# Kernel tuning notes

Hardware: AMD Instinct MI355X
Metric: run time of the kernel (lower is better)

## Reference

```python
import jax, jax.numpy as jnp
import numpy as np

B, S, D, DH, H, NCLS, VOCAB, L = 16, 512, 512, 512, 8, 10000, 32000, 6
HD = DH // H  # 64


def _norm(X, gamma, beta, axis):
    # torch.var is unbiased by default -> ddof=1
    mu = jnp.mean(X, axis=axis, keepdims=True)
    var = jnp.var(X, axis=axis, ddof=1, keepdims=True)
    return gamma * ((X - mu) / jnp.sqrt(var + 1e-8)) + beta


def _pos_table(s, d):
    pos = np.arange(s, dtype=np.float64)[:, None]
    i = np.arange(d, dtype=np.float64)[None, :]
    angle = pos / np.power(10000.0, (i - (i % 2)) / d)
    tab = np.where((np.arange(d)[None, :] % 2) == 0, np.sin(angle), np.cos(angle))
    return jnp.asarray(tab, dtype=jnp.float32)


def _encoder(x, p):
    b, s, d = x.shape

    def heads(w):
        y = x @ w.T                         # [B,S,DH]
        y = y.reshape(b, s, HD, H)          # interleaved split: channel c -> head c%8
        return jnp.transpose(y, (3, 0, 1, 2))  # [H,B,S,HD]

    q, k, v = heads(p['WQ']), heads(p['WK']), heads(p['WV'])
    # scaling uses d_k = x.shape[-1] = hidden_dim (not head_dim), as in source
    e = jnp.einsum('hbsd,hbtd->hbst', q, k) / jnp.sqrt(jnp.float32(d))
    e = _norm(e, p['ga'].reshape(H, 1, 1, 1), p['ba'].reshape(H, 1, 1, 1), axis=3)
    alpha = jax.nn.softmax(e, axis=3)
    head = jnp.einsum('hbst,hbtd->hbsd', alpha, v)      # [H,B,S,HD]
    a = jnp.transpose(head, (1, 2, 0, 3)).reshape(b, s, DH)  # cat(head[0..7], dim=2)
    attn = a @ p['WO']                                   # [B,S,D]
    x2 = _norm(attn + x, p['g1'], p['b1n'], axis=2)
    ff = jax.nn.relu(x2 @ p['W1'] + p['b1']) @ p['W2'] + p['b2']
    return _norm(ff + x2, p['g2'], p['b2n'], axis=2)


def setup_inputs() -> dict:
    key = jax.random.key(0)
    ks = jax.random.split(key, 16)
    sc = 0.05  # scale randn params for numerical stability across 6 layers
    return {
        'x': jax.random.randint(ks[0], (B, S), 0, VOCAB),
        'embedded_matrix': jax.random.normal(ks[1], (VOCAB, D), jnp.float32) * sc,
        'WQ': jax.random.normal(ks[2], (L, DH, D), jnp.float32) * sc,
        'WK': jax.random.normal(ks[3], (L, DH, D), jnp.float32) * sc,
        'WV': jax.random.normal(ks[4], (L, DH, D), jnp.float32) * sc,
        'WO': jax.random.normal(ks[5], (L, DH, D), jnp.float32) * sc,
        'W1': jax.random.normal(ks[6], (L, D, 4 * D), jnp.float32) * sc,
        'b1': jax.random.normal(ks[7], (L, 4 * D), jnp.float32) * sc,
        'W2': jax.random.normal(ks[8], (L, 4 * D, D), jnp.float32) * sc,
        'b2': jax.random.normal(ks[9], (L, D), jnp.float32) * sc,
        'gamma_a': jnp.ones((L, H, 1), jnp.float32),
        'beta_a': jnp.zeros((L, H, 1), jnp.float32),
        'gamma1': jnp.ones((L,), jnp.float32),
        'beta1': jnp.zeros((L,), jnp.float32),
        'gamma2': jnp.ones((L,), jnp.float32),
        'beta2': jnp.zeros((L,), jnp.float32),
        'V_e': jax.random.normal(ks[10], (D, 1), jnp.float32) * sc,
        'V_d': jax.random.normal(ks[11], (S, NCLS), jnp.float32) * sc,
        'gamma_f': jnp.ones((), jnp.float32),
        'beta_f': jnp.zeros((), jnp.float32),
    }


def reference(x, embedded_matrix, WQ, WK, WV, WO, W1, b1, W2, b2,
              gamma_a, beta_a, gamma1, beta1, gamma2, beta2,
              V_e, V_d, gamma_f, beta_f):
    x1 = embedded_matrix[x]                 # [B,S,D]
    x2 = x1 + _pos_table(S, D)
    acc = x1 + x2                           # input to encoder1 = x2 + x1
    params = {'WQ': WQ, 'WK': WK, 'WV': WV, 'WO': WO,
              'W1': W1, 'b1': b1, 'W2': W2, 'b2': b2,
              'ga': gamma_a, 'ba': beta_a,
              'g1': gamma1, 'b1n': beta1, 'g2': gamma2, 'b2n': beta2}

    def step(carry, p):
        out = _encoder(carry, p)
        # dense residual: next input = sum of ALL previous layer outputs + x1 + x2
        return carry + out, out

    _, outs = jax.lax.scan(step, acc, params)
    x8 = outs[-1]                           # [B,S,D]
    x9 = x8 @ V_e                           # [B,S,1]
    z = jnp.swapaxes(x9, 1, 2) @ V_d        # [B,1,NCLS]
    z = _norm(z, gamma_f, beta_f, axis=2)
    return jax.nn.softmax(z, axis=2).reshape(B, NCLS)
```

## Files before the change

### kernel.cpp

```cpp
#include <hip/hip_runtime.h>
#include <hip/hip_bf16.h>
#include <math.h>

#define N_TOK 8192
#define DMODEL 512
#define NHEAD 8
#define HDIM 64
#define SEQ 512
#define BATCH 16
#define FFDIM 2048
#define NLAYER 6
#define NCLS 10000
#define VD_SC 8

typedef unsigned short u16;
typedef __attribute__((ext_vector_type(8))) short bf16x8;
typedef __attribute__((ext_vector_type(8))) unsigned short u16x8;
typedef __attribute__((ext_vector_type(4))) unsigned short u16x4;
typedef __attribute__((ext_vector_type(4))) float f32x4;

__device__ __forceinline__ u16 f2b(float x) {
    unsigned int u = __float_as_uint(x);
    u += 0x7fffu + ((u >> 16) & 1u);
    return (u16)(u >> 16);
}

__device__ __forceinline__ void gl_lds16(const void* g, void* l) {
    __builtin_amdgcn_global_load_lds(
        (const __attribute__((address_space(1))) unsigned int*)g,
        (__attribute__((address_space(3))) unsigned int*)l, 16, 0, 0);
}

__global__ __launch_bounds__(512) void pos_kernel(float* __restrict__ pos) {
    const int i = threadIdx.x;
    const int s0 = blockIdx.x * 32;
    const double bse = pow(10000.0, -(double)(i & ~1) / 512.0);
    const double cb = cos(bse), sb = sin(bse);
    const double a0 = (double)s0 * bse;
    double sn = sin(a0), cs = cos(a0);
    const bool odd = i & 1;
    for (int k = 0; k < 32; ++k) {
        pos[(size_t)(s0 + k) * 512 + i] = (float)(odd ? cs : sn);
        const double ns = sn * cb + cs * sb;
        cs = cs * cb - sn * sb;
        sn = ns;
    }
}

__global__ __launch_bounds__(256) void embed_kernel(const int* __restrict__ xi,
        const float* __restrict__ emb, const float* __restrict__ pos,
        float* __restrict__ C, u16* __restrict__ Cb) {
    const int idx = blockIdx.x * 256 + threadIdx.x;
    const int n = idx >> 7, d4 = (idx & 127) << 2;
    const int row = xi[n];
    const int s = n & 511;
    const float4 e = *(const float4*)&emb[(size_t)row * 512 + d4];
    const float4 p = *(const float4*)&pos[(size_t)s * 512 + d4];
    float4 o;
    o.x = 2.f * e.x + p.x; o.y = 2.f * e.y + p.y;
    o.z = 2.f * e.z + p.z; o.w = 2.f * e.w + p.w;
    *(float4*)&C[(size_t)n * 512 + d4] = o;
    u16x4 ob = { f2b(o.x), f2b(o.y), f2b(o.z), f2b(o.w) };
    *(u16x4*)&Cb[(size_t)n * 512 + d4] = ob;
}

__global__ __launch_bounds__(256) void cvt3_kernel(const float* __restrict__ q,
        const float* __restrict__ k, const float* __restrict__ v,
        u16* __restrict__ dst) {
    const int i = blockIdx.x * 256 + threadIdx.x;
    const int l = i / 196608;
    const int rem = i - l * 196608;
    const int m = rem >> 16, r = rem & 65535;
    const float* src = (m == 0 ? q : (m == 1 ? k : v));
    const float4 vv = ((const float4*)src)[(size_t)l * 65536 + r];
    u16x4 o = { f2b(vv.x), f2b(vv.y), f2b(vv.z), f2b(vv.w) };
    *(u16x4*)&dst[(size_t)l * 786432 + (size_t)m * 262144 + (size_t)r * 4] = o;
}

__global__ __launch_bounds__(256) void tcvt_b16_kernel(const float* __restrict__ src,
        u16* __restrict__ dst, int Kd, int Nd) {
    __shared__ u16 t[64][65];
    const int k0 = blockIdx.x * 64, n0 = blockIdx.y * 64;
    const size_t off = (size_t)blockIdx.z * Kd * Nd;
    src += off; dst += off;
    const int cx = threadIdx.x & 63, r0 = threadIdx.x >> 6;
    #pragma unroll
    for (int i = 0; i < 16; ++i) {
        const int r = r0 * 16 + i;
        t[cx][r] = f2b(src[(size_t)(k0 + r) * Nd + n0 + cx]);
    }
    __syncthreads();
    #pragma unroll
    for (int i = 0; i < 16; ++i) {
        const int nn = r0 * 16 + i;
        dst[(size_t)(n0 + nn) * Kd + k0 + cx] = t[nn][cx];
    }
}

enum { EG_QKV3 = 0, EG_F32 = 1, EG_BIAS_F32 = 2, EG_BRELU_B16 = 3 };

template<int BM, int EPI>
__global__ __launch_bounds__(256)
void gemm_bf16(const u16* __restrict__ A, const u16* __restrict__ Bt,
               const float* __restrict__ bias, void* __restrict__ Cout,
               int N, int K) {
    constexpr int MF = BM / 32;
    __shared__ u16 As[BM * 64];
    __shared__ u16 Bs[128 * 64];
    const int tid = threadIdx.x, w = tid >> 6, l = tid & 63;
    const int g = l >> 4, c = l & 15;
    const int wm = w >> 1, wn = w & 1;
    const int bm = blockIdx.x * BM, bn = blockIdx.y * 128;
    const int sr = l >> 3, sc8 = l & 7;

    const f32x4 zero = {0.f, 0.f, 0.f, 0.f};
    f32x4 acc[MF][4];
    #pragma unroll
    for (int i = 0; i < MF; ++i)
        #pragma unroll
        for (int j = 0; j < 4; ++j) acc[i][j] = zero;

    for (int k0 = 0; k0 < K; k0 += 64) {
        __syncthreads();
        #pragma unroll
        for (int i = 0; i < MF; ++i) {
            const int rb = w * (BM / 4) + i * 8;
            const int r = rb + sr;
            const int ck = (sc8 ^ (r & 7)) * 8;
            gl_lds16(A + (size_t)(bm + r) * K + k0 + ck, &As[rb * 64]);
        }
        #pragma unroll
        for (int i = 0; i < 4; ++i) {
            const int rb = w * 32 + i * 8;
            const int r = rb + sr;
            const int ck = (sc8 ^ (r & 7)) * 8;
            gl_lds16(Bt + (size_t)(bn + r) * K + k0 + ck, &Bs[rb * 64]);
        }
        __syncthreads();
        #pragma unroll
        for (int ks = 0; ks < 2; ++ks) {
            bf16x8 af[MF], bfv[4];
            #pragma unroll
            for (int q = 0; q < MF; ++q) {
                const int ra = wm * (BM / 2) + q * 16 + c;
                af[q] = *(const bf16x8*)((const char*)As +
                        ((ra * 128 + ks * 64 + g * 16) ^ ((ra & 7) << 4)));
            }
            #pragma unroll
            for (int q = 0; q < 4; ++q) {
                const int rb2 = wn * 64 + q * 16 + c;
                bfv[q] = *(const bf16x8*)((const char*)Bs +
                        ((rb2 * 128 + ks * 64 + g * 16) ^ ((rb2 & 7) << 4)));
            }
            #pragma unroll
            for (int mf = 0; mf < MF; ++mf)
                #pragma unroll
                for (int nf = 0; nf < 4; ++nf)
                    acc[mf][nf] = __builtin_amdgcn_mfma_f32_16x16x32_bf16(
                        af[mf], bfv[nf], acc[mf][nf], 0, 0, 0);
        }
    }

    #pragma unroll
    for (int mf = 0; mf < MF; ++mf) {
        #pragma unroll
        for (int nf = 0; nf < 4; ++nf) {
            const int n  = bn + wn * 64 + nf * 16 + c;
            const int m0 = bm + wm * (BM / 2) + mf * 16 + g * 4;
            if (EPI == EG_QKV3) {
                u16* o = (u16*)Cout;
                const int seg = n >> 9, nn = n & 511;
                if (seg < 2) {
                    u16* dst = o + (size_t)seg * 4194304;
                    const size_t b0 = (size_t)(nn & 7) * N_TOK * 64 + (nn >> 3);
                    #pragma unroll
                    for (int r = 0; r < 4; ++r)
                        dst[b0 + (size_t)(m0 + r) * 64] = f2b(acc[mf][nf][r]);
                } else {
                    u16* dst = o + (size_t)2 * 4194304;
                    const int h = nn & 7, d = nn >> 3, bb = m0 >> 9, s0 = m0 & 511;
                    u16x4 pk = { f2b(acc[mf][nf][0]), f2b(acc[mf][nf][1]),
                                 f2b(acc[mf][nf][2]), f2b(acc[mf][nf][3]) };
                    *(u16x4*)&dst[((size_t)(h * 16 + bb) * 64 + d) * 512 + s0] = pk;
                }
            } else if (EPI == EG_F32) {
                float* o = (float*)Cout;
                #pragma unroll
                for (int r = 0; r < 4; ++r)
                    o[(size_t)(m0 + r) * N + n] = acc[mf][nf][r];
            } else if (EPI == EG_BIAS_F32) {
                float* o = (float*)Cout;
                const float bv = bias[n];
                #pragma unroll
                for (int r = 0; r < 4; ++r)
                    o[(size_t)(m0 + r) * N + n] = acc[mf][nf][r] + bv;
            } else {
                u16* o = (u16*)Cout;
                const float bv = bias[n];
                #pragma unroll
                for (int r = 0; r < 4; ++r)
                    o[(size_t)(m0 + r) * N + n] = f2b(fmaxf(acc[mf][nf][r] + bv, 0.f));
            }
        }
    }
}

__global__ __launch_bounds__(256, 2)
void attn_mfma(const u16* __restrict__ Qb, const u16* __restrict__ Kb,
               const u16* __restrict__ Vt, const float* __restrict__ ga,
               const float* __restrict__ ba, u16* __restrict__ A, float scale) {
    __shared__ __align__(16) u16 KV[2][8192];
    __shared__ __align__(16) u16 P[4][2][16][136];
    const int bid = blockIdx.x;
    const int hb = bid & 127, qc = bid >> 7;
    const int h = hb >> 4, b = hb & 15;
    const int tid = threadIdx.x, w = tid >> 6, l = tid & 63;
    const int g = l >> 4, c = l & 15;
    const float gah = ga[h], bah = ba[h];
    const size_t qkbase = ((size_t)h * N_TOK + (size_t)b * SEQ) * 64;
    const size_t vtbase = ((size_t)(h * 16 + b)) * 64 * 512;
    const int q0 = qc * 64 + w * 16;
    const int swz = (c & 7) << 4;
    const int srK = l >> 3, scK = l & 7;
    const int srV = l >> 4, scV = l & 15;

    #pragma unroll
    for (int i = 0; i < 4; ++i) {
        const int rb = w * 32 + i * 8;
        const int r = rb + srK;
        gl_lds16(Kb + qkbase + (size_t)r * 64 + (scK ^ (r & 7)) * 8,
                 &KV[0][rb * 64]);
    }
    const u16* qrow = Qb + qkbase + (size_t)(q0 + c) * 64;
    const bf16x8 qf0 = *(const bf16x8*)(qrow + g * 8);
    const bf16x8 qf1 = *(const bf16x8*)(qrow + 32 + g * 8);
    __syncthreads();

    f32x4 acc[32];
    int buf = 0;
    #pragma unroll
    for (int ch = 0; ch < 4; ++ch) {
        if (ch < 3) {
            #pragma unroll
            for (int i = 0; i < 4; ++i) {
                const int rb = w * 32 + i * 8;
                const int r = rb + srK;
                gl_lds16(Kb + qkbase + (size_t)((ch + 1) * 128 + r) * 64 + (scK ^ (r & 7)) * 8,
                         &KV[buf ^ 1][rb * 64]);
            }
        }
        const char* kb = (const char*)&KV[buf][0];
        #pragma unroll
        for (int tt = 0; tt < 8; ++tt) {
            const int r = tt * 16 + c;
            const int sx = (r & 7) << 4;
            const char* rowp = kb + r * 128;
            const bf16x8 kf0 = *(const bf16x8*)(rowp + ((g * 16) ^ sx));
            const bf16x8 kf1 = *(const bf16x8*)(rowp + ((64 + g * 16) ^ sx));
            f32x4 z = {0.f, 0.f, 0.f, 0.f};
            z = __builtin_amdgcn_mfma_f32_16x16x32_bf16(kf0, qf0, z, 0, 0, 0);
            z = __builtin_amdgcn_mfma_f32_16x16x32_bf16(kf1, qf1, z, 0, 0, 0);
            acc[ch * 8 + tt] = z;
        }
        if (ch < 3) { __syncthreads(); buf ^= 1; }
    }

    #pragma unroll
    for (int i = 0; i < 4; ++i) {
        const int db = w * 16 + i * 4;
        const int d = db + srV;
        gl_lds16(Vt + vtbase + (size_t)d * 512 + (scV ^ (d & 7)) * 8,
                 &KV[0][db * 128]);
    }

    float sm = 0.f, sq = 0.f;
    #pragma unroll
    for (int t = 0; t < 32; ++t)
        #pragma unroll
        for (int r = 0; r < 4; ++r) {
            const float v = acc[t][r];
            sm += v; sq = fmaf(v, v, sq);
        }
    sm += __shfl_xor(sm, 16); sm += __shfl_xor(sm, 32);
    sq += __shfl_xor(sq, 16); sq += __shfl_xor(sq, 32);

    const float LOG2E = 1.4426950408889634f;
    const float S  = sm * scale;
    const float Qq = sq * scale * scale;
    const float mu = S * (1.f / 512.f);
    const float var = (Qq - 512.f * mu * mu) * (1.f / 511.f);
    const float rg = rsqrtf(var + 1e-8f) * gah;
    const float A2 = scale * rg * LOG2E;
    const float B2 = (bah - mu * rg) * LOG2E;

    __syncthreads();

    float se = 0.f;
    f32x4 oacc[4];
    #pragma unroll
    for (int dt = 0; dt < 4; ++dt) oacc[dt] = (f32x4){0.f, 0.f, 0.f, 0.f};

    int vbuf = 0;
    #pragma unroll
    for (int ch = 0; ch < 4; ++ch) {
        if (ch < 3) {
            #pragma unroll
            for (int i = 0; i < 4; ++i) {
                const int db = w * 16 + i * 4;
                const int d = db + srV;
                gl_lds16(Vt + vtbase + (size_t)d * 512 + (ch + 1) * 128 + (scV ^ (d & 7)) * 8,
                         &KV[vbuf ^ 1][db * 128]);
            }
        }
        char* pbase = (char*)&P[w][ch & 1][0][0];
        #pragma unroll
        for (int tt = 0; tt < 8; ++tt) {
            const int t = ch * 8 + tt;
            float p0 = exp2f(fmaf(acc[t][0], A2, B2));
            float p1 = exp2f(fmaf(acc[t][1], A2, B2));
            float p2 = exp2f(fmaf(acc[t][2], A2, B2));
            float p3 = exp2f(fmaf(acc[t][3], A2, B2));
            se += (p0 + p1) + (p2 + p3);
            u16x4 pk = { f2b(p0), f2b(p1), f2b(p2), f2b(p3) };
            *(u16x4*)(pbase + c * 272 + ((tt * 32 + g * 8) ^ swz)) = pk;
        }
        const char* vb = (const char*)&KV[vbuf][0];
        #pragma unroll
        for (int ks = 0; ks < 4; ++ks) {
            const bf16x8 pf = *(const bf16x8*)(pbase + c * 272 + ((ks * 64 + g * 16) ^ swz));
            #pragma unroll
            for (int dt = 0; dt < 4; ++dt) {
                const int d = dt * 16 + c;
                const bf16x8 vf = *(const bf16x8*)(vb + d * 256 +
                        ((ks * 64 + g * 16) ^ ((d & 7) << 4)));
                oacc[dt] = __builtin_amdgcn_mfma_f32_16x16x32_bf16(pf, vf, oacc[dt], 0, 0, 0);
            }
        }
        if (ch < 3) { __syncthreads(); vbuf ^= 1; }
    }

    se += __shfl_xor(se, 16); se += __shfl_xor(se, 32);
    const float inv = 1.f / se;
    float iv[4];
    #pragma unroll
    for (int r = 0; r < 4; ++r) iv[r] = __shfl(inv, g * 4 + r);
    #pragma unroll
    for (int dt = 0; dt < 4; ++dt)
        #pragma unroll
        for (int r = 0; r < 4; ++r)
            A[((size_t)(b * 512 + q0 + g * 4 + r)) * 512 + h * 64 + dt * 16 + c] =
                f2b(oacc[dt][r] * iv[r]);
}

__global__ __launch_bounds__(256)
void ln_res_kernel(const float* __restrict__ X, const float* __restrict__ R,
                   const float* __restrict__ gp, const float* __restrict__ bp,
                   int lidx, float* __restrict__ Y, u16* __restrict__ Yb,
                   float* __restrict__ Cacc, u16* __restrict__ Cb) {
    const int tid = threadIdx.x, w = tid >> 6, l = tid & 63;
    const size_t row = (size_t)blockIdx.x * 4 + w;
    const float g = gp[lidx], bb = bp[lidx];
    const float* x = X + row * 512;
    const float* r = R + row * 512;
    float v[8];
    const float4 a0 = *(const float4*)&x[l * 8], a1 = *(const float4*)&x[l * 8 + 4];
    const float4 r0 = *(const float4*)&r[l * 8], r1 = *(const float4*)&r[l * 8 + 4];
    v[0] = a0.x + r0.x; v[1] = a0.y + r0.y; v[2] = a0.z + r0.z; v[3] = a0.w + r0.w;
    v[4] = a1.x + r1.x; v[5] = a1.y + r1.y; v[6] = a1.z + r1.z; v[7] = a1.w + r1.w;
    float s = 0.f, sq = 0.f;
    #pragma unroll
    for (int i = 0; i < 8; ++i) { s += v[i]; sq = fmaf(v[i], v[i], sq); }
    #pragma unroll
    for (int o = 1; o < 64; o <<= 1) { s += __shfl_xor(s, o); sq += __shfl_xor(sq, o); }
    const float mu   = s * (1.f / 512.f);
    const float var  = (sq - 512.f * mu * mu) * (1.f / 511.f);
    const float rstd = rsqrtf(var + 1e-8f);
    float y[8];
    #pragma unroll
    for (int i = 0; i < 8; ++i) y[i] = fmaf((v[i] - mu) * rstd, g, bb);
    if (Y) {
        *(float4*)&Y[row * 512 + l * 8]     = *(float4*)&y[0];
        *(float4*)&Y[row * 512 + l * 8 + 4] = *(float4*)&y[4];
    }
    if (Yb) {
        u16x8 yb;
        #pragma unroll
        for (int i = 0; i < 8; ++i) yb[i] = f2b(y[i]);
        *(u16x8*)&Yb[row * 512 + l * 8] = yb;
    }
    if (Cacc) {
        float cv[8];
        float4 c0 = *(float4*)&Cacc[row * 512 + l * 8];
        float4 c1 = *(float4*)&Cacc[row * 512 + l * 8 + 4];
        cv[0] = c0.x + y[0]; cv[1] = c0.y + y[1]; cv[2] = c0.z + y[2]; cv[3] = c0.w + y[3];
        cv[4] = c1.x + y[4]; cv[5] = c1.y + y[5]; cv[6] = c1.z + y[6]; cv[7] = c1.w + y[7];
        *(float4*)&Cacc[row * 512 + l * 8]     = *(float4*)&cv[0];
        *(float4*)&Cacc[row * 512 + l * 8 + 4] = *(float4*)&cv[4];
        u16x8 cb;
        #pragma unroll
        for (int i = 0; i < 8; ++i) cb[i] = f2b(cv[i]);
        *(u16x8*)&Cb[row * 512 + l * 8] = cb;
    }
}

__global__ __launch_bounds__(256)
void fin_ve_kernel(const float* __restrict__ X8, const float* __restrict__ Ve,
                   float* __restrict__ x9) {
    const int tid = threadIdx.x, w = tid >> 6, l = tid & 63;
    const size_t row = (size_t)blockIdx.x * 4 + w;
    const float* x = X8 + row * 512;
    float s = 0.f;
    #pragma unroll
    for (int i = 0; i < 8; ++i) s = fmaf(x[l * 8 + i], Ve[l * 8 + i], s);
    #pragma unroll
    for (int o = 1; o < 64; o <<= 1) s += __shfl_xor(s, o);
    if (l == 0) x9[row] = s;
}

__global__ __launch_bounds__(256)
void fin_vd_part(const float* __restrict__ x9, const float* __restrict__ Vd,
                 float* __restrict__ zp) {
    __shared__ float xs[16][64];
    const int tid = threadIdx.x;
    const int c = blockIdx.x * 256 + tid;
    const int sc = blockIdx.y, s0 = sc * 64;
    #pragma unroll
    for (int p = 0; p < 4; ++p) {
        const int idx = p * 256 + tid;
        xs[idx >> 6][idx & 63] = x9[(idx >> 6) * 512 + s0 + (idx & 63)];
    }
    __syncthreads();
    float acc[16];
    #pragma unroll
    for (int b = 0; b < 16; ++b) acc[b] = 0.f;
    if (c < NCLS) {
        for (int s = 0; s < 64; ++s) {
            const float vd = Vd[(size_t)(s0 + s) * NCLS + c];
            #pragma unroll
            for (int b = 0; b < 16; ++b) acc[b] = fmaf(xs[b][s], vd, acc[b]);
        }
    }
    #pragma unroll
    for (int b = 0; b < 16; ++b)
        zp[((size_t)sc * 16 + b) * 10240 + c] = acc[b];
}

__global__ __launch_bounds__(256)
void fin_sm_kernel(const float* __restrict__ zp, const float* __restrict__ gp,
                   const float* __restrict__ bp, float* __restrict__ out) {
    __shared__ float zs[NCLS];
    __shared__ float red[4];
    __shared__ float red2[4];
    const int b = blockIdx.x, tid = threadIdx.x, w = tid >> 6, l = tid & 63;
    float s = 0.f, sq = 0.f;
    for (int i = tid; i < NCLS; i += 256) {
        float v = 0.f;
        #pragma unroll
        for (int sc = 0; sc < VD_SC; ++sc)
            v += zp[((size_t)sc * 16 + b) * 10240 + i];
        zs[i] = v; s += v; sq = fmaf(v, v, sq);
    }
    #pragma unroll
    for (int o = 1; o < 64; o <<= 1) { s += __shfl_xor(s, o); sq += __shfl_xor(sq, o); }
    if (l == 0) { red[w] = s; red2[w] = sq; }
    __syncthreads();
    s  = red[0] + red[1] + red[2] + red[3];
    sq = red2[0] + red2[1] + red2[2] + red2[3];
    const float mu   = s / 10000.f;
    const float var  = (sq - 10000.f * mu * mu) / 9999.f;
    const float rstd = rsqrtf(var + 1e-8f);
    const float g = gp[0], be = bp[0];
    __syncthreads();
    float mx = -1e30f;
    for (int i = tid; i < NCLS; i += 256) {
        const float e = fmaf((zs[i] - mu) * rstd, g, be);
        zs[i] = e; mx = fmaxf(mx, e);
    }
    #pragma unroll
    for (int o = 1; o < 64; o <<= 1) mx = fmaxf(mx, __shfl_xor(mx, o));
    if (l == 0) red[w] = mx;
    __syncthreads();
    mx = fmaxf(fmaxf(red[0], red[1]), fmaxf(red[2], red[3]));
    float es = 0.f;
    for (int i = tid; i < NCLS; i += 256) {
        const float p = expf(zs[i] - mx);
        zs[i] = p; es += p;
    }
    #pragma unroll
    for (int o = 1; o < 64; o <<= 1) es += __shfl_xor(es, o);
    if (l == 0) red2[w] = es;
    __syncthreads();
    es = red2[0] + red2[1] + red2[2] + red2[3];
    const float inv = 1.f / es;
    for (int i = tid; i < NCLS; i += 256) out[(size_t)b * NCLS + i] = zs[i] * inv;
}

extern "C" void kernel_launch(void* const* d_in, const int* in_sizes, int n_in,
                              void* d_out, int out_size, void* d_ws, size_t ws_size,
                              hipStream_t stream) {
    (void)in_sizes; (void)n_in; (void)out_size; (void)ws_size;
    const int*   xi  = (const int*)d_in[0];
    const float* emb = (const float*)d_in[1];
    const float* WQ  = (const float*)d_in[2];
    const float* WK  = (const float*)d_in[3];
    const float* WV  = (const float*)d_in[4];
    const float* WO  = (const float*)d_in[5];
    const float* W1  = (const float*)d_in[6];
    const float* b1  = (const float*)d_in[7];
    const float* W2  = (const float*)d_in[8];
    const float* b2  = (const float*)d_in[9];
    const float* ga  = (const float*)d_in[10];
    const float* ba  = (const float*)d_in[11];
    const float* g1  = (const float*)d_in[12];
    const float* be1 = (const float*)d_in[13];
    const float* g2  = (const float*)d_in[14];
    const float* be2 = (const float*)d_in[15];
    const float* Ve  = (const float*)d_in[16];
    const float* Vd  = (const float*)d_in[17];
    const float* gf  = (const float*)d_in[18];
    const float* bf  = (const float*)d_in[19];
    float* out = (float*)d_out;

    float* ws  = (float*)d_ws;
    float* pos = ws;
    float* C   = pos + 262144;
    float* X2  = C   + 4194304;
    float* OUT = X2  + 4194304;
    float* PF  = OUT + 4194304;
    u16* ub = (u16*)(PF + 4194304);
    u16* Cb  = ub;  ub += 4194304;
    u16* X2b = ub;  ub += 4194304;
    u16* Qbf = ub;  ub += 4194304;
    u16* Kbf = ub;  ub += 4194304;
    u16* Vtb = ub;  ub += 4194304;
    u16* Abf = ub;  ub += 4194304;
    u16* Hb  = Qbf;
    float* zp = (float*)Vtb;
    u16* WQKVb = ub; ub += 4718592;
    u16* WOt = ub; ub += 1572864;
    u16* W1t = ub; ub += 6291456;
    u16* W2t = ub; ub += 6291456;
    float* x9 = (float*)ub;

    pos_kernel<<<16, 512, 0, stream>>>(pos);
    embed_kernel<<<4096, 256, 0, stream>>>(xi, emb, pos, C, Cb);

    cvt3_kernel<<<4608, 256, 0, stream>>>(WQ, WK, WV, WQKVb);
    tcvt_b16_kernel<<<dim3(8,  8, 6), 256, 0, stream>>>(WO, WOt, 512, 512);
    tcvt_b16_kernel<<<dim3(8, 32, 6), 256, 0, stream>>>(W1, W1t, 512, 2048);
    tcvt_b16_kernel<<<dim3(32, 8, 6), 256, 0, stream>>>(W2, W2t, 2048, 512);

    const float scale = 1.0f / sqrtf(512.0f);

    for (int l = 0; l < NLAYER; ++l) {
        const u16* wqkv = WQKVb + (size_t)l * 786432;
        const u16* wo = WOt + (size_t)l * 262144;
        const u16* w1 = W1t + (size_t)l * 1048576;
        const u16* w2 = W2t + (size_t)l * 1048576;

        gemm_bf16<128, EG_QKV3>     <<<dim3(64, 12), 256, 0, stream>>>(Cb, wqkv, nullptr, Qbf, 1536, 512);
        attn_mfma                   <<<1024, 256, 0, stream>>>(Qbf, Kbf, Vtb, ga + l*8, ba + l*8, Abf, scale);
        gemm_bf16<64, EG_F32>       <<<dim3(128, 4), 256, 0, stream>>>(Abf, wo, nullptr, PF, 512, 512);
        ln_res_kernel               <<<2048, 256, 0, stream>>>(PF, C, g1, be1, l, X2, X2b, nullptr, nullptr);
        gemm_bf16<128, EG_BRELU_B16><<<dim3(64, 16), 256, 0, stream>>>(X2b, w1, b1 + l*2048, Hb, 2048, 512);
        gemm_bf16<64, EG_BIAS_F32>  <<<dim3(128, 4), 256, 0, stream>>>(Hb, w2, b2 + l*512, PF, 512, 2048);
        ln_res_kernel               <<<2048, 256, 0, stream>>>(PF, X2, g2, be2, l,
                                                               (l == NLAYER - 1) ? OUT : nullptr,
                                                               nullptr, C, Cb);
    }

    fin_ve_kernel<<<2048, 256, 0, stream>>>(OUT, Ve, x9);
    fin_vd_part<<<dim3(40, VD_SC), 256, 0, stream>>>(x9, Vd, zp);
    fin_sm_kernel<<<16, 256, 0, stream>>>(zp, gf, bf, out);
}
```

Baseline: 1.033 ms.

## Double-buffer GEMM LDS loads and permute Q/K weight rows for contiguous head layout

The bf16 GEMM now keeps two LDS buffers and prefetches the next K-tile with direct-to-LDS loads while computing the current one. It uses explicit vmcnt waits and raw s_barrier calls in place of the two __syncthreads per iteration. Separately, the Q and K weight rows are permuted at conversion time so each head's 64 channels are contiguous. This lets the QKV epilogue write row-major [token,512] rows instead of scattered strided stores, and attention reads Q/K with a 512 stride. The cost is twice the LDS per block, which may lower occupancy, and the hand-tuned waitcnt values depend on the exact number of loads issued per stage.

```diff
diff --git a/kernel.cpp b/kernel.cpp
--- a/kernel.cpp
+++ b/kernel.cpp
@@ -71,10 +71,12 @@
     const int l = i / 196608;
     const int rem = i - l * 196608;
     const int m = rem >> 16, r = rem & 65535;
+    const int j = r >> 7, col4 = r & 127;
+    const int srow = (m == 2) ? j : ((j >> 6) | ((j & 63) << 3));
     const float* src = (m == 0 ? q : (m == 1 ? k : v));
-    const float4 vv = ((const float4*)src)[(size_t)l * 65536 + r];
+    const float4 vv = ((const float4*)src)[(size_t)l * 65536 + srow * 128 + col4];
     u16x4 o = { f2b(vv.x), f2b(vv.y), f2b(vv.z), f2b(vv.w) };
-    *(u16x4*)&dst[(size_t)l * 786432 + (size_t)m * 262144 + (size_t)r * 4] = o;
+    *(u16x4*)&dst[(size_t)l * 786432 + (size_t)m * 262144 + (size_t)(j * 128 + col4) * 4] = o;
 }
 
 __global__ __launch_bounds__(256) void tcvt_b16_kernel(const float* __restrict__ src,
@@ -105,8 +107,8 @@
                const float* __restrict__ bias, void* __restrict__ Cout,
                int N, int K) {
     constexpr int MF = BM / 32;
-    __shared__ u16 As[BM * 64];
-    __shared__ u16 Bs[128 * 64];
+    __shared__ u16 As[2][BM * 64];
+    __shared__ u16 Bs[2][128 * 64];
     const int tid = threadIdx.x, w = tid >> 6, l = tid & 63;
     const int g = l >> 4, c = l & 15;
     const int wm = w >> 1, wn = w & 1;
@@ -120,36 +122,39 @@
         #pragma unroll
         for (int j = 0; j < 4; ++j) acc[i][j] = zero;
 
-    for (int k0 = 0; k0 < K; k0 += 64) {
-        __syncthreads();
+    auto stage = [&](int buf, int k0) {
         #pragma unroll
         for (int i = 0; i < MF; ++i) {
             const int rb = w * (BM / 4) + i * 8;
             const int r = rb + sr;
             const int ck = (sc8 ^ (r & 7)) * 8;
-            gl_lds16(A + (size_t)(bm + r) * K + k0 + ck, &As[rb * 64]);
+            gl_lds16(A + (size_t)(bm + r) * K + k0 + ck, &As[buf][rb * 64]);
         }
         #pragma unroll
         for (int i = 0; i < 4; ++i) {
             const int rb = w * 32 + i * 8;
             const int r = rb + sr;
             const int ck = (sc8 ^ (r & 7)) * 8;
-            gl_lds16(Bt + (size_t)(bn + r) * K + k0 + ck, &Bs[rb * 64]);
-        }
-        __syncthreads();
+            gl_lds16(Bt + (size_t)(bn + r) * K + k0 + ck, &Bs[buf][rb * 64]);
+        }
+    };
+
+    auto compute = [&](int buf) {
+        const char* Ab = (const char*)&As[buf][0];
+        const char* Bb = (const char*)&Bs[buf][0];
         #pragma unroll
         for (int ks = 0; ks < 2; ++ks) {
             bf16x8 af[MF], bfv[4];
             #pragma unroll
             for (int q = 0; q < MF; ++q) {
                 const int ra = wm * (BM / 2) + q * 16 + c;
-                af[q] = *(const bf16x8*)((const char*)As +
+                af[q] = *(const bf16x8*)(Ab +
                         ((ra * 128 + ks * 64 + g * 16) ^ ((ra & 7) << 4)));
             }
             #pragma unroll
             for (int q = 0; q < 4; ++q) {
                 const int rb2 = wn * 64 + q * 16 + c;
-                bfv[q] = *(const bf16x8*)((const char*)Bs +
+                bfv[q] = *(const bf16x8*)(Bb +
                         ((rb2 * 128 + ks * 64 + g * 16) ^ ((rb2 & 7) << 4)));
             }
             #pragma unroll
@@ -159,7 +164,26 @@
                     acc[mf][nf] = __builtin_amdgcn_mfma_f32_16x16x32_bf16(
                         af[mf], bfv[nf], acc[mf][nf], 0, 0, 0);
         }
-    }
+    };
+
+    stage(0, 0);
+    int cur = 0;
+    for (int k0 = 0; k0 + 64 < K; k0 += 64) {
+        stage(cur ^ 1, k0 + 64);
+        __builtin_amdgcn_sched_barrier(0);
+        if (MF == 4) asm volatile("s_waitcnt vmcnt(8)" ::: "memory");
+        else         asm volatile("s_waitcnt vmcnt(6)" ::: "memory");
+        __builtin_amdgcn_s_barrier();
+        __builtin_amdgcn_sched_barrier(0);
+        compute(cur);
+        __builtin_amdgcn_sched_barrier(0);
+        __builtin_amdgcn_s_barrier();
+        cur ^= 1;
+    }
+    asm volatile("s_waitcnt vmcnt(0)" ::: "memory");
+    __builtin_amdgcn_s_barrier();
+    __builtin_amdgcn_sched_barrier(0);
+    compute(cur);
 
     #pragma unroll
     for (int mf = 0; mf < MF; ++mf) {
@@ -172,10 +196,9 @@
                 const int seg = n >> 9, nn = n & 511;
                 if (seg < 2) {
                     u16* dst = o + (size_t)seg * 4194304;
-                    const size_t b0 = (size_t)(nn & 7) * N_TOK * 64 + (nn >> 3);
                     #pragma unroll
                     for (int r = 0; r < 4; ++r)
-                        dst[b0 + (size_t)(m0 + r) * 64] = f2b(acc[mf][nf][r]);
+                        dst[(size_t)(m0 + r) * 512 + nn] = f2b(acc[mf][nf][r]);
                 } else {
                     u16* dst = o + (size_t)2 * 4194304;
                     const int h = nn & 7, d = nn >> 3, bb = m0 >> 9, s0 = m0 & 511;
@@ -217,7 +240,8 @@
     const int tid = threadIdx.x, w = tid >> 6, l = tid & 63;
     const int g = l >> 4, c = l & 15;
     const float gah = ga[h], bah = ba[h];
-    const size_t qkbase = ((size_t)h * N_TOK + (size_t)b * SEQ) * 64;
+    const size_t tok0 = (size_t)b * SEQ;
+    const int hoff = h * 64;
     const size_t vtbase = ((size_t)(h * 16 + b)) * 64 * 512;
     const int q0 = qc * 64 + w * 16;
     const int swz = (c & 7) << 4;
@@ -228,10 +252,10 @@
     for (int i = 0; i < 4; ++i) {
         const int rb = w * 32 + i * 8;
         const int r = rb + srK;
-        gl_lds16(Kb + qkbase + (size_t)r * 64 + (scK ^ (r & 7)) * 8,
+        gl_lds16(Kb + (tok0 + r) * 512 + hoff + (scK ^ (r & 7)) * 8,
                  &KV[0][rb * 64]);
     }
-    const u16* qrow = Qb + qkbase + (size_t)(q0 + c) * 64;
+    const u16* qrow = Qb + (tok0 + q0 + c) * 512 + hoff;
     const bf16x8 qf0 = *(const bf16x8*)(qrow + g * 8);
     const bf16x8 qf1 = *(const bf16x8*)(qrow + 32 + g * 8);
     __syncthreads();
@@ -245,7 +269,7 @@
             for (int i = 0; i < 4; ++i) {
                 const int rb = w * 32 + i * 8;
                 const int r = rb + srK;
-                gl_lds16(Kb + qkbase + (size_t)((ch + 1) * 128 + r) * 64 + (scK ^ (r & 7)) * 8,
+                gl_lds16(Kb + (tok0 + (ch + 1) * 128 + r) * 512 + hoff + (scK ^ (r & 7)) * 8,
                          &KV[buf ^ 1][rb * 64]);
             }
         }
```

Result: faster. 938.5 us (-9.2%).
